# Kernel optimization log

Hardware: AMD Instinct MI355X
Metric: run time of the kernel (lower is better)

## Reference

```python
import jax, jax.numpy as jnp
import numpy as np

EPS = 1e-8

def rmsnorm(x, w):
    norm = jax.lax.rsqrt(jnp.mean(x * x, axis=-1, keepdims=True) + EPS)
    return x * norm * w

def setup_inputs() -> dict:
    key = jax.random.key(0)
    ks = jax.random.split(key, 10)
    B, L, D, S = 8, 4096, 1024, 256
    sD = 1.0 / np.sqrt(D)
    sS = 1.0 / np.sqrt(S)
    return {
        "x": jax.random.normal(ks[0], (B, L, D), jnp.float32),
        "w_norm": jnp.ones((D,), jnp.float32),
        "W_in": jax.random.normal(ks[1], (D, 3 * S), jnp.float32) * sD,
        "b_in": jnp.zeros((3 * S,), jnp.float32),
        "W_x": jax.random.normal(ks[2], (S, S), jnp.float32) * sS,
        "b_x": jnp.zeros((S,), jnp.float32),
        "W_dt": jax.random.normal(ks[3], (S, S), jnp.float32) * sS,
        "b_dt": jnp.zeros((S,), jnp.float32),
        "W_out": jax.random.normal(ks[4], (S, D), jnp.float32) * sS,
        "b_out": jnp.zeros((D,), jnp.float32),
    }

def reference(x, w_norm, W_in, b_in, W_x, b_x, W_dt, b_dt, W_out, b_out):
    # MambaLikeBlock forward (dropout=0 / eval mode)
    residual = x
    xn = rmsnorm(x, w_norm)
    uzg = xn @ W_in + b_in                       # [B,L,3S]
    S = uzg.shape[-1] // 3
    u, z, g = uzg[..., :S], uzg[..., S:2 * S], uzg[..., 2 * S:]
    # per-step projections are time-independent -> precompute for all t
    ut = jnp.tanh(u @ W_x + b_x)                 # [B,L,S]
    dt = jax.nn.sigmoid(z @ W_dt + b_dt)         # [B,L,S]

    def step(h, inp):
        u_t, dt_t = inp
        h = (1.0 - dt_t) * h + dt_t * u_t
        return h, h

    h0 = jnp.zeros(ut.shape[::2][::-1][:0] + (ut.shape[0], ut.shape[2]), ut.dtype)  # [B,S]
    _, hs = jax.lax.scan(step, h0, (ut.transpose(1, 0, 2), dt.transpose(1, 0, 2)))
    hs = hs.transpose(1, 0, 2)                   # [B,L,S]
    y = hs * jax.nn.sigmoid(g)
    y = y @ W_out + b_out                        # [B,L,D]
    return residual + y
```

## Files before the change

### kernel.cpp

```cpp
#include <hip/hip_runtime.h>
#include <hip/hip_bf16.h>

#define BB 8
#define LL 4096
#define DD 1024
#define SS 256
#define NTOK (BB * LL)
#define CCH 64
#define TCH (LL / CCH)

typedef short bf16x8 __attribute__((ext_vector_type(8)));
typedef float f32x4 __attribute__((ext_vector_type(4)));

__device__ __forceinline__ float bfu(unsigned short v) {
  union { unsigned int i; float f; } x;
  x.i = ((unsigned int)v) << 16;
  return x.f;
}

__device__ __forceinline__ void gl_lds16(const __hip_bfloat16* g, void* l) {
  __builtin_amdgcn_global_load_lds(
      (const __attribute__((address_space(1))) unsigned int*)g,
      (__attribute__((address_space(3))) unsigned int*)l, 16, 0, 0);
}

__global__ __launch_bounds__(256) void prep_rms(const float* __restrict__ x,
                                                const float* __restrict__ wn,
                                                __hip_bfloat16* __restrict__ xn) {
  const size_t row = blockIdx.x;
  const int t = threadIdx.x;
  const float4 xv = reinterpret_cast<const float4*>(x + row * DD)[t];
  const float4 wv = reinterpret_cast<const float4*>(wn)[t];
  float ss = xv.x * xv.x + xv.y * xv.y + xv.z * xv.z + xv.w * xv.w;
#pragma unroll
  for (int m = 32; m >= 1; m >>= 1) ss += __shfl_xor(ss, m);
  __shared__ float red[4];
  if ((t & 63) == 0) red[t >> 6] = ss;
  __syncthreads();
  const float tot = red[0] + red[1] + red[2] + red[3];
  const float r = rsqrtf(tot * (1.0f / DD) + 1e-8f);
  union { ushort4 u; __hip_bfloat16 h[4]; } o;
  o.h[0] = __float2bfloat16(xv.x * wv.x * r);
  o.h[1] = __float2bfloat16(xv.y * wv.y * r);
  o.h[2] = __float2bfloat16(xv.z * wv.z * r);
  o.h[3] = __float2bfloat16(xv.w * wv.w * r);
  reinterpret_cast<ushort4*>(xn + row * DD)[t] = o.u;
}

__global__ __launch_bounds__(256) void convT4(
    const float* __restrict__ W0, const float* __restrict__ W1,
    const float* __restrict__ W2, const float* __restrict__ W3,
    __hip_bfloat16* __restrict__ T0, __hip_bfloat16* __restrict__ T1,
    __hip_bfloat16* __restrict__ T2, __hip_bfloat16* __restrict__ T3) {
  const int seg = blockIdx.y;
  const int K = (seg == 0) ? DD : SS;
  const int Nw = (seg == 0) ? 768 : (seg == 3) ? DD : SS;
  const float* W = (seg == 0) ? W0 : (seg == 1) ? W1 : (seg == 2) ? W2 : W3;
  __hip_bfloat16* T = (seg == 0) ? T0 : (seg == 1) ? T1 : (seg == 2) ? T2 : T3;
  const int idx = blockIdx.x * 256 + threadIdx.x;
  if (idx >= K * Nw) return;
  const int k = idx / Nw, n = idx % Nw;
  T[(size_t)n * K + k] = __float2bfloat16(W[idx]);
}

template <int EPI>
__global__ __launch_bounds__(256) void gemm_bf16(
    const __hip_bfloat16* __restrict__ A, int lda,
    const __hip_bfloat16* __restrict__ BT,
    const float* __restrict__ bias,
    void* __restrict__ Cptr, int ldc,
    const float* __restrict__ resid,
    int K) {
  __shared__ __align__(16) __hip_bfloat16 As[128][64];
  __shared__ __align__(16) __hip_bfloat16 Bs[128][64];

  const int t = threadIdx.x;
  const int bm = blockIdx.x, bn = blockIdx.y;
  const int wave = t >> 6, lane = t & 63;
  const int wr = (wave >> 1) * 64;
  const int wc = (wave & 1) * 64;
  const int lr = lane & 15;
  const int kg = lane >> 4;

  const int g_row = wave * 32 + (lane >> 3);
  const int g_col = (lane & 7) * 8;
  const __hip_bfloat16* Ab = A + (size_t)(bm * 128 + g_row) * lda + g_col;
  const __hip_bfloat16* Bb = BT + (size_t)(bn * 128 + g_row) * K + g_col;
  char* lAs = (char*)(&As[0][0]) + (size_t)(wave * 32) * 128;
  char* lBs = (char*)(&Bs[0][0]) + (size_t)(wave * 32) * 128;

  f32x4 acc[4][4] = {};

  for (int k0 = 0; k0 < K; k0 += 64) {
    __syncthreads();
#pragma unroll
    for (int p = 0; p < 4; ++p) {
      gl_lds16(Ab + (size_t)(p * 8) * lda + k0, lAs + p * 1024);
      gl_lds16(Bb + (size_t)(p * 8) * K + k0, lBs + p * 1024);
    }
    __syncthreads();
#pragma unroll
    for (int kk = 0; kk < 64; kk += 32) {
      bf16x8 af[4], bfr[4];
#pragma unroll
      for (int m = 0; m < 4; ++m)
        af[m] = *reinterpret_cast<const bf16x8*>(&As[wr + m * 16 + lr][kk + kg * 8]);
#pragma unroll
      for (int n = 0; n < 4; ++n)
        bfr[n] = *reinterpret_cast<const bf16x8*>(&Bs[wc + n * 16 + lr][kk + kg * 8]);
#pragma unroll
      for (int m = 0; m < 4; ++m)
#pragma unroll
        for (int n = 0; n < 4; ++n)
          acc[m][n] = __builtin_amdgcn_mfma_f32_16x16x32_bf16(bfr[n], af[m],
                                                              acc[m][n], 0, 0, 0);
    }
  }

  const int row0 = bm * 128 + wr + lr;
  const int col0 = bn * 128 + wc + kg * 4;
#pragma unroll
  for (int m = 0; m < 4; ++m) {
    const int row = row0 + m * 16;
#pragma unroll
    for (int n = 0; n < 4; ++n) {
      const int colb = col0 + n * 16;
      const float4 bv = *reinterpret_cast<const float4*>(&bias[colb]);
      float v0 = acc[m][n][0] + bv.x;
      float v1 = acc[m][n][1] + bv.y;
      float v2 = acc[m][n][2] + bv.z;
      float v3 = acc[m][n][3] + bv.w;
      if (EPI == 3) {
        const size_t off = (size_t)row * ldc + colb;
        const float4 rv = *reinterpret_cast<const float4*>(&resid[off]);
        float4 ov;
        ov.x = v0 + rv.x; ov.y = v1 + rv.y; ov.z = v2 + rv.z; ov.w = v3 + rv.w;
        *reinterpret_cast<float4*>(&((float*)Cptr)[off]) = ov;
      } else {
        if (EPI == 1) {
          v0 = tanhf(v0); v1 = tanhf(v1); v2 = tanhf(v2); v3 = tanhf(v3);
        } else if (EPI == 2) {
          v0 = 1.f / (1.f + expf(-v0)); v1 = 1.f / (1.f + expf(-v1));
          v2 = 1.f / (1.f + expf(-v2)); v3 = 1.f / (1.f + expf(-v3));
        }
        union { ushort4 u; __hip_bfloat16 h[4]; } o;
        o.h[0] = __float2bfloat16(v0); o.h[1] = __float2bfloat16(v1);
        o.h[2] = __float2bfloat16(v2); o.h[3] = __float2bfloat16(v3);
        *reinterpret_cast<ushort4*>(
            &((__hip_bfloat16*)Cptr)[(size_t)row * ldc + colb]) = o.u;
      }
    }
  }
}

__global__ __launch_bounds__(128) void scan_phase_a(
    const __hip_bfloat16* __restrict__ ut,
    const __hip_bfloat16* __restrict__ dtb,
    float* __restrict__ h0s, float* __restrict__ As) {
  const int bc = blockIdx.x;
  const int b = bc / CCH, c = bc % CCH;
  const int ch = threadIdx.x * 2;
  const size_t base = ((size_t)b * LL + (size_t)c * TCH) * SS + ch;
  float h0 = 0.f, h1 = 0.f, A0 = 1.f, A1 = 1.f;
#pragma unroll 8
  for (int t = 0; t < TCH; ++t) {
    const ushort2 uu = *reinterpret_cast<const ushort2*>(ut + base + (size_t)t * SS);
    const ushort2 dd = *reinterpret_cast<const ushort2*>(dtb + base + (size_t)t * SS);
    const float d0 = bfu(dd.x), d1 = bfu(dd.y);
    h0 = fmaf(d0, bfu(uu.x) - h0, h0);
    h1 = fmaf(d1, bfu(uu.y) - h1, h1);
    A0 *= (1.f - d0);
    A1 *= (1.f - d1);
  }
  const size_t o = (size_t)bc * SS + ch;
  *reinterpret_cast<float2*>(h0s + o) = make_float2(h0, h1);
  *reinterpret_cast<float2*>(As + o) = make_float2(A0, A1);
}

__global__ __launch_bounds__(256) void scan_phase_b(
    const float* __restrict__ h0s, const float* __restrict__ As,
    float* __restrict__ hins) {
  const int b = blockIdx.x;
  const int s = threadIdx.x;
  float hin = 0.f;
#pragma unroll 8
  for (int c = 0; c < CCH; ++c) {
    const size_t idx = ((size_t)b * CCH + c) * SS + s;
    hins[idx] = hin;
    hin = fmaf(As[idx], hin, h0s[idx]);
  }
}

__global__ __launch_bounds__(128) void scan_phase_c(
    const __hip_bfloat16* __restrict__ ut,
    const __hip_bfloat16* __restrict__ dtb,
    const __hip_bfloat16* __restrict__ gz,
    const float* __restrict__ hins,
    __hip_bfloat16* __restrict__ hsg) {
  const int bc = blockIdx.x;
  const int b = bc / CCH, c = bc % CCH;
  const int ch = threadIdx.x * 2;
  const size_t rowbase = (size_t)b * LL + (size_t)c * TCH;
  const float2 hv = *reinterpret_cast<const float2*>(hins + (size_t)bc * SS + ch);
  float h0 = hv.x, h1 = hv.y;
#pragma unroll 8
  for (int t = 0; t < TCH; ++t) {
    const size_t row = rowbase + t;
    const ushort2 uu = *reinterpret_cast<const ushort2*>(ut + row * SS + ch);
    const ushort2 dd = *reinterpret_cast<const ushort2*>(dtb + row * SS + ch);
    const ushort2 gg = *reinterpret_cast<const ushort2*>(gz + row * 768 + ch);
    h0 = fmaf(bfu(dd.x), bfu(uu.x) - h0, h0);
    h1 = fmaf(bfu(dd.y), bfu(uu.y) - h1, h1);
    union { ushort2 u; __hip_bfloat16 h[2]; } o;
    o.h[0] = __float2bfloat16(h0 / (1.f + expf(-bfu(gg.x))));
    o.h[1] = __float2bfloat16(h1 / (1.f + expf(-bfu(gg.y))));
    *reinterpret_cast<ushort2*>(hsg + row * SS + ch) = o.u;
  }
}

extern "C" void kernel_launch(void* const* d_in, const int* in_sizes, int n_in,
                              void* d_out, int out_size, void* d_ws, size_t ws_size,
                              hipStream_t stream) {
  const float* x      = (const float*)d_in[0];
  const float* w_norm = (const float*)d_in[1];
  const float* W_in   = (const float*)d_in[2];
  const float* b_in   = (const float*)d_in[3];
  const float* W_x    = (const float*)d_in[4];
  const float* b_x    = (const float*)d_in[5];
  const float* W_dt   = (const float*)d_in[6];
  const float* b_dt   = (const float*)d_in[7];
  const float* W_out  = (const float*)d_in[8];
  const float* b_out  = (const float*)d_in[9];
  float* out = (float*)d_out;

  char* w = (char*)d_ws;
  __hip_bfloat16* xn  = (__hip_bfloat16*)w;
  __hip_bfloat16* ut  = (__hip_bfloat16*)w;
  __hip_bfloat16* dtb = (__hip_bfloat16*)(w + (size_t)NTOK * SS * 2);
  w += (size_t)NTOK * DD * 2;
  __hip_bfloat16* uzg = (__hip_bfloat16*)w;  w += (size_t)NTOK * 768 * 2;
  __hip_bfloat16* WinT  = (__hip_bfloat16*)w;  w += (size_t)768 * DD * 2;
  __hip_bfloat16* WxT   = (__hip_bfloat16*)w;  w += (size_t)SS * SS * 2;
  __hip_bfloat16* WdtT  = (__hip_bfloat16*)w;  w += (size_t)SS * SS * 2;
  __hip_bfloat16* WoutT = (__hip_bfloat16*)w;  w += (size_t)DD * SS * 2;
  float* h0s  = (float*)w;  w += (size_t)BB * CCH * SS * 4;
  float* As   = (float*)w;  w += (size_t)BB * CCH * SS * 4;
  float* hins = (float*)w;  w += (size_t)BB * CCH * SS * 4;
  (void)ws_size; (void)n_in; (void)in_sizes; (void)out_size;

  convT4<<<dim3((DD * 768 + 255) / 256, 4), 256, 0, stream>>>(
      W_in, W_x, W_dt, W_out, WinT, WxT, WdtT, WoutT);

  prep_rms<<<NTOK, 256, 0, stream>>>(x, w_norm, xn);

  gemm_bf16<0><<<dim3(NTOK / 128, 768 / 128), 256, 0, stream>>>(
      xn, DD, WinT, b_in, uzg, 768, nullptr, DD);

  gemm_bf16<1><<<dim3(NTOK / 128, SS / 128), 256, 0, stream>>>(
      uzg, 768, WxT, b_x, ut, SS, nullptr, SS);
  gemm_bf16<2><<<dim3(NTOK / 128, SS / 128), 256, 0, stream>>>(
      uzg + SS, 768, WdtT, b_dt, dtb, SS, nullptr, SS);

  scan_phase_a<<<BB * CCH, 128, 0, stream>>>(ut, dtb, h0s, As);
  scan_phase_b<<<BB, 256, 0, stream>>>(h0s, As, hins);
  scan_phase_c<<<BB * CCH, 128, 0, stream>>>(ut, dtb, uzg + 2 * SS, hins, ut);

  gemm_bf16<3><<<dim3(NTOK / 128, DD / 128), 256, 0, stream>>>(
      ut, SS, WoutT, b_out, out, DD, x, SS);
}
```

Before: 297.8 us.

## Double-buffer GEMM LDS tiles and XOR-swizzle layout to avoid bank conflicts

The bf16 MFMA GEMM now keeps two LDS buffers per operand. It prefetches the next K tile with global_load_lds while computing on the current one, and uses one barrier per iteration instead of two. The global source column group is XOR-swizzled by row, and the fragment reads undo the swizzle, to cut LDS bank conflicts on the 16-byte reads. LDS use per block doubles to 64KB, which may lower occupancy, and correctness depends on the barrier waiting for the async LDS loads.

```diff
diff --git a/kernel.cpp b/kernel.cpp
--- a/kernel.cpp
+++ b/kernel.cpp
@@ -71,8 +71,8 @@
     void* __restrict__ Cptr, int ldc,
     const float* __restrict__ resid,
     int K) {
-  __shared__ __align__(16) __hip_bfloat16 As[128][64];
-  __shared__ __align__(16) __hip_bfloat16 Bs[128][64];
+  __shared__ __align__(16) char ldsA[2][128 * 128];
+  __shared__ __align__(16) char ldsB[2][128 * 128];
 
   const int t = threadIdx.x;
   const int bm = blockIdx.x, bn = blockIdx.y;
@@ -81,33 +81,48 @@
   const int wc = (wave & 1) * 64;
   const int lr = lane & 15;
   const int kg = lane >> 4;
-
-  const int g_row = wave * 32 + (lane >> 3);
-  const int g_col = (lane & 7) * 8;
-  const __hip_bfloat16* Ab = A + (size_t)(bm * 128 + g_row) * lda + g_col;
-  const __hip_bfloat16* Bb = BT + (size_t)(bn * 128 + g_row) * K + g_col;
-  char* lAs = (char*)(&As[0][0]) + (size_t)(wave * 32) * 128;
-  char* lBs = (char*)(&Bs[0][0]) + (size_t)(wave * 32) * 128;
+  const int rsw = lr & 7;
+
+  const int srow = lane >> 3;
+  const int sg = (lane & 7) ^ srow;
+  const int g_row = wave * 32 + srow;
+  const __hip_bfloat16* Ab = A + (size_t)(bm * 128 + g_row) * lda + sg * 8;
+  const __hip_bfloat16* Bb = BT + (size_t)(bn * 128 + g_row) * K + sg * 8;
 
   f32x4 acc[4][4] = {};
 
-  for (int k0 = 0; k0 < K; k0 += 64) {
-    __syncthreads();
-#pragma unroll
-    for (int p = 0; p < 4; ++p) {
-      gl_lds16(Ab + (size_t)(p * 8) * lda + k0, lAs + p * 1024);
-      gl_lds16(Bb + (size_t)(p * 8) * K + k0, lBs + p * 1024);
-    }
-    __syncthreads();
-#pragma unroll
-    for (int kk = 0; kk < 64; kk += 32) {
+#define STAGE(d, koff)                                                       \
+  {                                                                          \
+    _Pragma("unroll") for (int p = 0; p < 4; ++p) {                          \
+      gl_lds16(Ab + (size_t)(p * 8) * lda + (koff),                          \
+               ldsA[d] + (wave * 32 + p * 8) * 128);                         \
+      gl_lds16(Bb + (size_t)(p * 8) * K + (koff),                            \
+               ldsB[d] + (wave * 32 + p * 8) * 128);                         \
+    }                                                                        \
+  }
+
+  const int NT = K >> 6;
+  STAGE(0, 0);
+  __syncthreads();
+
+  for (int ti = 0; ti < NT; ++ti) {
+    const int cur = ti & 1;
+    if (ti + 1 < NT) STAGE(cur ^ 1, (ti + 1) * 64);
+#pragma unroll
+    for (int kh = 0; kh < 2; ++kh) {
       bf16x8 af[4], bfr[4];
 #pragma unroll
-      for (int m = 0; m < 4; ++m)
-        af[m] = *reinterpret_cast<const bf16x8*>(&As[wr + m * 16 + lr][kk + kg * 8]);
-#pragma unroll
-      for (int n = 0; n < 4; ++n)
-        bfr[n] = *reinterpret_cast<const bf16x8*>(&Bs[wc + n * 16 + lr][kk + kg * 8]);
+      for (int m = 0; m < 4; ++m) {
+        const int row = wr + m * 16 + lr;
+        const int slot = (kg + kh * 4) ^ rsw;
+        af[m] = *reinterpret_cast<const bf16x8*>(ldsA[cur] + row * 128 + slot * 16);
+      }
+#pragma unroll
+      for (int n = 0; n < 4; ++n) {
+        const int row = wc + n * 16 + lr;
+        const int slot = (kg + kh * 4) ^ rsw;
+        bfr[n] = *reinterpret_cast<const bf16x8*>(ldsB[cur] + row * 128 + slot * 16);
+      }
 #pragma unroll
       for (int m = 0; m < 4; ++m)
 #pragma unroll
@@ -115,7 +130,9 @@
           acc[m][n] = __builtin_amdgcn_mfma_f32_16x16x32_bf16(bfr[n], af[m],
                                                               acc[m][n], 0, 0, 0);
     }
-  }
+    __syncthreads();
+  }
+#undef STAGE
 
   const int row0 = bm * 128 + wr + lr;
   const int col0 = bn * 128 + wc + kg * 4;
```

After: 281.8 us. 1.06x faster.
